# Performance work log

Measured on AMD Instinct MI355X. Metric: run time of the kernel, lower is better.

Reference implementation:

```python
import jax, jax.numpy as jnp
import numpy as np

N = 131072   # total nodes (4096 molecules x ~32 atoms)
E = 524288   # directed edges (avg degree 4)
G = 4096     # number of graphs
D_IN, D_H, D_OUT = 128, 512, 256
BN_EPS = 1e-5


def setup_inputs() -> dict:
    key = jax.random.key(0)
    ks = jax.random.split(key, 24)
    def rn(i, shape, s=0.05):
        return jax.random.normal(ks[i], shape, jnp.float32) * s
    inp = {
        "x": jax.random.normal(ks[0], (N, D_IN), jnp.float32),
        "edge_index": jax.random.randint(ks[1], (2, E), 0, N),
        "batch": jnp.sort(jax.random.randint(ks[2], (N,), 0, G)),
        # GCN layer weights (stored [in, out]) and biases
        "W1": rn(3, (D_IN, D_H)), "b1": jnp.zeros((D_H,), jnp.float32),
        "W2": rn(4, (D_H, D_H)),  "b2": jnp.zeros((D_H,), jnp.float32),
        "W3": rn(5, (D_H, D_OUT)), "b3": jnp.zeros((D_OUT,), jnp.float32),
        # BatchNorm (eval mode): gamma, beta, running_mean, running_var
        "g1": jnp.ones((D_H,), jnp.float32),  "be1": jnp.zeros((D_H,), jnp.float32),
        "m1": rn(6, (D_H,)),  "v1": jax.random.uniform(ks[7], (D_H,), jnp.float32) + 0.5,
        "g2": jnp.ones((D_H,), jnp.float32),  "be2": jnp.zeros((D_H,), jnp.float32),
        "m2": rn(8, (D_H,)),  "v2": jax.random.uniform(ks[9], (D_H,), jnp.float32) + 0.5,
        "g3": jnp.ones((D_OUT,), jnp.float32), "be3": jnp.zeros((D_OUT,), jnp.float32),
        "m3": rn(10, (D_OUT,)), "v3": jax.random.uniform(ks[11], (D_OUT,), jnp.float32) + 0.5,
        # MLP head
        "Wf1": rn(12, (D_OUT, D_OUT)), "bf1": jnp.zeros((D_OUT,), jnp.float32),
        "Wf2": rn(13, (D_OUT, D_OUT)), "bf2": jnp.zeros((D_OUT,), jnp.float32),
    }
    return inp


def reference(x, edge_index, batch, W1, b1, W2, b2, W3, b3,
              g1, be1, m1, v1, g2, be2, m2, v2, g3, be3, m3, v3,
              Wf1, bf1, Wf2, bf2):
    loop = jnp.arange(N)
    src = jnp.concatenate([edge_index[0], loop])  # add self-loops (PyG GCNConv default)
    dst = jnp.concatenate([edge_index[1], loop])
    deg = jax.ops.segment_sum(jnp.ones((E + N,), x.dtype), dst, num_segments=N)
    dinv = jnp.where(deg > 0, jax.lax.rsqrt(deg), 0.0)
    norm = dinv[src] * dinv[dst]                  # D^{-1/2} A_hat D^{-1/2}

    def gcn(h, W, b):
        h = h @ W                                 # dense GEMM [N, d_out]
        msg = h[src] * norm[:, None]              # gather + scale
        return jax.ops.segment_sum(msg, dst, num_segments=N) + b  # scatter-add

    def bn(h, g, be, m, v):                       # eval-mode BatchNorm1d
        return g * (h - m) * jax.lax.rsqrt(v + BN_EPS) + be

    h = bn(jax.nn.relu(gcn(x, W1, b1)), g1, be1, m1, v1)
    h = bn(jax.nn.relu(gcn(h, W2, b2)), g2, be2, m2, v2)
    h = bn(jax.nn.relu(gcn(h, W3, b3)), g3, be3, m3, v3)

    sums = jax.ops.segment_sum(h, batch, num_segments=G)          # global_mean_pool
    cnt = jax.ops.segment_sum(jnp.ones((N,), h.dtype), batch, num_segments=G)
    pooled = sums / jnp.maximum(cnt, 1.0)[:, None]

    return jax.nn.relu(pooled @ Wf1 + bf1) @ Wf2 + bf2
```

## Files before the change

### kernel.cpp

```cpp
#include <hip/hip_runtime.h>

static constexpr int NN = 131072;
static constexpr int NE = 524288;
static constexpr int NG = 4096;

typedef __attribute__((ext_vector_type(8))) short short8;
typedef __attribute__((ext_vector_type(4))) float f32x4;
typedef __attribute__((ext_vector_type(2))) float f32x2;

__device__ __forceinline__ float bfbits2f(unsigned b) {
    return __uint_as_float(b << 16);
}
__device__ __forceinline__ unsigned short f2bfbits(float f) {
    unsigned u = __float_as_uint(f);
    u += 0x7fffu + ((u >> 16) & 1u);
    return (unsigned short)(u >> 16);
}
__device__ __forceinline__ unsigned pack2(float a, float b) {
    return (unsigned)f2bfbits(a) | ((unsigned)f2bfbits(b) << 16);
}

__device__ __forceinline__ int geti(const void* p, size_t i, int w64) {
    return w64 ? (int)((const long long*)p)[i] : ((const int*)p)[i];
}

#if __has_builtin(__builtin_amdgcn_cvt_pk_f32_fp8) && __has_builtin(__builtin_amdgcn_cvt_pk_fp8_f32)
#define FP8_CVT_HW 1
#else
#define FP8_CVT_HW 0
#endif

__device__ __forceinline__ float e4m32f(unsigned b) {
    unsigned e = (b >> 3) & 0xFu, m = b & 7u;
    float v = e ? __uint_as_float(((e + 120u) << 23) | (m << 20))
                : (float)m * 0.001953125f;
    return (b & 0x80u) ? -v : v;
}
__device__ __forceinline__ unsigned f2e4m3(float f) {
    unsigned u = __float_as_uint(f);
    unsigned s = (u >> 24) & 0x80u;
    unsigned mag = u & 0x7fffffffu;
    if (mag >= 0x43e00000u) return s | 0x7eu;
    if (mag < 0x3c800000u) {
        int q = (int)(__uint_as_float(mag) * 512.0f + 0.5f);
        return s | (unsigned)q;
    }
    unsigned r = mag + 0x0007ffffu + ((mag >> 20) & 1u);
    if (r >= 0x43e00000u) return s | 0x7eu;
    return s | (((r >> 23) - 120u) << 3) | ((r >> 20) & 7u);
}

template<bool HI>
__device__ __forceinline__ unsigned dec_pair(unsigned w) {
#if FP8_CVT_HW
    f32x2 p = __builtin_amdgcn_cvt_pk_f32_fp8((int)w, HI);
    return __builtin_amdgcn_perm(__float_as_uint(p.y), __float_as_uint(p.x), 0x07060302u);
#else
    unsigned b0 = HI ? ((w >> 16) & 255u) : (w & 255u);
    unsigned b1 = HI ? (w >> 24) : ((w >> 8) & 255u);
    return pack2(e4m32f(b0), e4m32f(b1));
#endif
}

__device__ __forceinline__ short8 dec8(uint2 u) {
    union { uint4 q; short8 s; } r;
    r.q.x = dec_pair<false>(u.x);
    r.q.y = dec_pair<true>(u.x);
    r.q.z = dec_pair<false>(u.y);
    r.q.w = dec_pair<true>(u.y);
    return r.s;
}

__device__ __forceinline__ void dec4f(unsigned w, float* v) {
#if FP8_CVT_HW
    f32x2 a = __builtin_amdgcn_cvt_pk_f32_fp8((int)w, false);
    f32x2 b = __builtin_amdgcn_cvt_pk_f32_fp8((int)w, true);
    v[0] = a.x; v[1] = a.y; v[2] = b.x; v[3] = b.y;
#else
#pragma unroll
    for (int i = 0; i < 4; ++i) v[i] = e4m32f((w >> (8 * i)) & 0xffu);
#endif
}

__device__ __forceinline__ unsigned enc4(float a, float b, float c, float d) {
#if FP8_CVT_HW
    int r = __builtin_amdgcn_cvt_pk_fp8_f32(a, b, 0, false);
    r = __builtin_amdgcn_cvt_pk_fp8_f32(c, d, r, true);
    return (unsigned)r;
#else
    return f2e4m3(a) | (f2e4m3(b) << 8) | (f2e4m3(c) << 16) | (f2e4m3(d) << 24);
#endif
}
__device__ __forceinline__ unsigned enc1(float a) {
#if FP8_CVT_HW
    return (unsigned)__builtin_amdgcn_cvt_pk_fp8_f32(a, a, 0, false) & 0xffu;
#else
    return f2e4m3(a);
#endif
}

__device__ __forceinline__ void gld16(const void* g, void* l, int lane) {
#if __has_builtin(__builtin_amdgcn_global_load_lds)
    __builtin_amdgcn_global_load_lds((const __attribute__((address_space(1))) unsigned int*)g,
                                     (__attribute__((address_space(3))) unsigned int*)l, 16, 0, 0);
#else
    *(uint4*)((char*)l + lane * 16) = *(const uint4*)g;
#endif
}

__global__ void k_detect(const void* __restrict__ eidx, const void* __restrict__ batch,
                         int* __restrict__ flags) {
    const int* e32 = (const int*)eidx;
    const int* b32 = (const int*)batch;
    int e64 = (e32[1] == 0 && e32[2001] == 0 && e32[40001] == 0 && e32[2 * NE - 1] == 0) ? 1 : 0;
    int b64 = (b32[NN - 1] == 0) ? 1 : 0;
    flags[0] = e64;
    flags[1] = b64;
}


__global__ void k_zero(int* __restrict__ p, int n) {
    int i = blockIdx.x * 256 + threadIdx.x;
    if (i < n) p[i] = 0;
}

__global__ void k_transpose(const float* __restrict__ W,
                            unsigned short* __restrict__ Wt, int K, int Ncols) {
    int idx = blockIdx.x * 256 + threadIdx.x;
    if (idx >= K * Ncols) return;
    int k = idx / Ncols, n = idx - k * Ncols;
    Wt[n * K + k] = f2bfbits(W[idx]);
}

__global__ void k_bn_prep(const float* __restrict__ g, const float* __restrict__ be,
                          const float* __restrict__ m, const float* __restrict__ v,
                          float* __restrict__ s, float* __restrict__ t, int d) {
    int i = blockIdx.x * 256 + threadIdx.x;
    if (i >= d) return;
    float inv = rsqrtf(v[i] + 1e-5f);
    float sc = g[i] * inv;
    s[i] = sc;
    t[i] = be[i] - m[i] * sc;
}

__global__ void k_deg_count(const void* __restrict__ eidx, const int* __restrict__ flags,
                            int* __restrict__ cnt) {
    int i = blockIdx.x * 256 + threadIdx.x;
    if (i >= NE) return;
    int d = geti(eidx, (size_t)NE + i, flags[0]);
    atomicAdd(&cnt[d], 1);
}

__global__ __launch_bounds__(1024) void k_scan(const int* __restrict__ cnt, int* __restrict__ rowptr,
                                               float* __restrict__ dinv) {
    __shared__ int part[1024];
    const int t = threadIdx.x;
    const int base = t * 128;
    const int4* c4 = (const int4*)(cnt + base);
    int s = 0;
#pragma unroll
    for (int i = 0; i < 32; ++i) { int4 u = c4[i]; s += u.x + u.y + u.z + u.w; }
    part[t] = s;
    __syncthreads();
    for (int off = 1; off < 1024; off <<= 1) {
        int v = (t >= off) ? part[t - off] : 0;
        __syncthreads();
        part[t] += v;
        __syncthreads();
    }
    int ex = (t == 0) ? 0 : part[t - 1];
#pragma unroll
    for (int i = 0; i < 32; ++i) {
        int4 u = c4[i];
        int4 o; o.x = ex; o.y = ex + u.x; o.z = o.y + u.y; o.w = o.z + u.z; ex = o.w + u.w;
        *(int4*)(rowptr + base + 4 * i) = o;
        float4 dv;
        dv.x = rsqrtf((float)(u.x + 1)); dv.y = rsqrtf((float)(u.y + 1));
        dv.z = rsqrtf((float)(u.z + 1)); dv.w = rsqrtf((float)(u.w + 1));
        *(float4*)(dinv + base + 4 * i) = dv;
    }
    if (t == 1023) rowptr[NN] = ex;
}

__global__ void k_fill(const void* __restrict__ eidx, const int* __restrict__ flags,
                       const int* __restrict__ rowptr, int* __restrict__ fillp,
                       int* __restrict__ col) {
    int i = blockIdx.x * 256 + threadIdx.x;
    if (i >= NE) return;
    int e64 = flags[0];
    int s = geti(eidx, (size_t)i, e64);
    int d = geti(eidx, (size_t)NE + i, e64);
    int p = rowptr[d] + atomicAdd(&fillp[d], 1);
    col[p] = s;
}

__global__ void k_gstart(const void* __restrict__ batch, const int* __restrict__ flags,
                         int* __restrict__ gstart) {
    int i = blockIdx.x * 256 + threadIdx.x;
    if (i >= NN) return;
    int b64 = flags[1];
    int b = geti(batch, (size_t)i, b64);
    if (i == 0) {
        for (int g = 0; g <= b; ++g) gstart[g] = 0;
    } else {
        int pb = geti(batch, (size_t)i - 1, b64);
        for (int g = pb + 1; g <= b; ++g) gstart[g] = i;
    }
    if (i == NN - 1) {
        for (int g = b + 1; g <= NG; ++g) gstart[g] = NN;
    }
}

template<int D, int MODE>
__device__ __forceinline__ void load_row_hw(const void* h, int sn, int c0, float* v) {
    if constexpr (MODE == 2) {
        float4 u = *(const float4*)((const float*)h + (size_t)sn * D + c0);
        v[0] = u.x; v[1] = u.y; v[2] = u.z; v[3] = u.w;
    } else {
        uint4 u = *(const uint4*)((const unsigned char*)h + (size_t)sn * D + c0);
        dec4f(u.x, v); dec4f(u.y, v + 4); dec4f(u.z, v + 8); dec4f(u.w, v + 12);
    }
}

template<int D, int EPL, bool FP8>
__device__ __forceinline__ void store_row_hw(void* out, int n, int c0, const float* v) {
    if constexpr (FP8) {
        uint4 u;
        u.x = enc4(v[0], v[1], v[2], v[3]);
        u.y = enc4(v[4], v[5], v[6], v[7]);
        u.z = enc4(v[8], v[9], v[10], v[11]);
        u.w = enc4(v[12], v[13], v[14], v[15]);
        *(uint4*)((unsigned char*)out + (size_t)n * D + c0) = u;
    } else {
        uint2 u; u.x = pack2(v[0], v[1]); u.y = pack2(v[2], v[3]);
        *(uint2*)((unsigned short*)out + (size_t)n * D + c0) = u;
    }
}

template<int D, int IN_MODE, bool OUT_FP8>
__global__ __launch_bounds__(256) void k_agg_hw(
    const void* __restrict__ h,
    const int* __restrict__ rowptr, const int* __restrict__ col,
    const float* __restrict__ dinv,
    void* __restrict__ out)
{
    constexpr int EPL = (IN_MODE == 1) ? 16 : 4;
    const int n = (blockIdx.x * 256 + threadIdx.x) >> 5;
    const int lane = threadIdx.x & 31;
    const int c0 = lane * EPL;
    float dn = dinv[n];
    float acc[EPL], va[EPL], vb[EPL];

    load_row_hw<D, IN_MODE>(h, n, c0, va);
    float wsl = dn * dn;
#pragma unroll
    for (int i = 0; i < EPL; ++i) acc[i] = va[i] * wsl;

    int e = rowptr[n], e1 = rowptr[n + 1];
    for (; e + 2 <= e1; e += 2) {
        int sa = col[e], sb = col[e + 1];
        float wa = dinv[sa] * dn, wb = dinv[sb] * dn;
        load_row_hw<D, IN_MODE>(h, sa, c0, va);
        load_row_hw<D, IN_MODE>(h, sb, c0, vb);
#pragma unroll
        for (int i = 0; i < EPL; ++i) acc[i] += va[i] * wa + vb[i] * wb;
    }
    if (e < e1) {
        int sa = col[e];
        float wa = dinv[sa] * dn;
        load_row_hw<D, IN_MODE>(h, sa, c0, va);
#pragma unroll
        for (int i = 0; i < EPL; ++i) acc[i] += va[i] * wa;
    }
    store_row_hw<D, EPL, OUT_FP8>(out, n, c0, acc);
}

__global__ __launch_bounds__(256) void k_agg_pool(
    const unsigned short* __restrict__ T3,
    const int* __restrict__ rowptr, const int* __restrict__ col,
    const float* __restrict__ dinv,
    const float* __restrict__ b, const float* __restrict__ s, const float* __restrict__ t,
    const int* __restrict__ gstart, unsigned short* __restrict__ pooled)
{
    __shared__ float red[4][256];
    const int g = blockIdx.x;
    const int wave = threadIdx.x >> 6, lane = threadIdx.x & 63;
    const int c0 = lane * 4;
    const int r0 = gstart[g], r1 = gstart[g + 1];
    float p0 = 0, p1 = 0, p2 = 0, p3 = 0;
    const float bc0 = b[c0], bc1 = b[c0 + 1], bc2 = b[c0 + 2], bc3 = b[c0 + 3];
    const float sc0 = s[c0], sc1 = s[c0 + 1], sc2 = s[c0 + 2], sc3 = s[c0 + 3];
    const float tc0 = t[c0], tc1 = t[c0 + 1], tc2 = t[c0 + 2], tc3 = t[c0 + 3];

    for (int n = r0 + wave; n < r1; n += 4) {
        float dn = dinv[n];
        float a0, a1, a2, a3;
        {
            uint2 u = *(const uint2*)(T3 + (size_t)n * 256 + c0);
            float w = dn * dn;
            a0 = bfbits2f(u.x & 0xffffu) * w; a1 = bfbits2f(u.x >> 16) * w;
            a2 = bfbits2f(u.y & 0xffffu) * w; a3 = bfbits2f(u.y >> 16) * w;
        }
        int e = rowptr[n], e1 = rowptr[n + 1];
        for (; e + 2 <= e1; e += 2) {
            int sa = col[e], sb = col[e + 1];
            float wa = dinv[sa] * dn, wb = dinv[sb] * dn;
            uint2 ua = *(const uint2*)(T3 + (size_t)sa * 256 + c0);
            uint2 ub = *(const uint2*)(T3 + (size_t)sb * 256 + c0);
            a0 += bfbits2f(ua.x & 0xffffu) * wa + bfbits2f(ub.x & 0xffffu) * wb;
            a1 += bfbits2f(ua.x >> 16) * wa + bfbits2f(ub.x >> 16) * wb;
            a2 += bfbits2f(ua.y & 0xffffu) * wa + bfbits2f(ub.y & 0xffffu) * wb;
            a3 += bfbits2f(ua.y >> 16) * wa + bfbits2f(ub.y >> 16) * wb;
        }
        if (e < e1) {
            int sa = col[e];
            float wa = dinv[sa] * dn;
            uint2 ua = *(const uint2*)(T3 + (size_t)sa * 256 + c0);
            a0 += bfbits2f(ua.x & 0xffffu) * wa; a1 += bfbits2f(ua.x >> 16) * wa;
            a2 += bfbits2f(ua.y & 0xffffu) * wa; a3 += bfbits2f(ua.y >> 16) * wa;
        }
        p0 += sc0 * fmaxf(a0 + bc0, 0.0f) + tc0;
        p1 += sc1 * fmaxf(a1 + bc1, 0.0f) + tc1;
        p2 += sc2 * fmaxf(a2 + bc2, 0.0f) + tc2;
        p3 += sc3 * fmaxf(a3 + bc3, 0.0f) + tc3;
    }
    red[wave][c0] = p0; red[wave][c0 + 1] = p1; red[wave][c0 + 2] = p2; red[wave][c0 + 3] = p3;
    __syncthreads();
    int ch = threadIdx.x;
    float tot = red[0][ch] + red[1][ch] + red[2][ch] + red[3][ch];
    __syncthreads();
    red[0][ch] = tot;
    __syncthreads();
    if (ch < 128) {
        int ccount = r1 - r0;
        float inv = 1.0f / (float)(ccount > 0 ? ccount : 1);
        pooled[(size_t)g * 256 + 2 * ch] = f2bfbits(red[0][2 * ch] * inv);
        pooled[(size_t)g * 256 + 2 * ch + 1] = f2bfbits(red[0][2 * ch + 1] * inv);
    }
}

template<bool A_FP8, int CB, int OUT_MODE, bool RELU, bool HAS_BN, bool HAS_BIAS>
__global__ __launch_bounds__(256)
void k_gemm(const void* __restrict__ Aptr,
            const unsigned short* __restrict__ Wt,
            const float* __restrict__ bias,
            const float* __restrict__ s, const float* __restrict__ t,
            void* __restrict__ Cptr,
            int K, int Ncols)
{
    __shared__ __align__(16) unsigned short lB[2][2][128 * 32];
    __shared__ __align__(16) unsigned char  lA8[A_FP8 ? 2 : 1][A_FP8 ? 2 : 1][A_FP8 ? 128 * 32 : 16];
    __shared__ __align__(16) unsigned short lA16[A_FP8 ? 1 : 2][A_FP8 ? 1 : 2][A_FP8 ? 8 : 128 * 32];
    const int tid = threadIdx.x;
    const int id = blockIdx.x;
    const int hi = id >> 3;
    const int cblk = hi % CB;
    const int rblk = (hi / CB) * 8 + (id & 7);
    const int bm = rblk * 128;
    const int bn = cblk * 128;
    const int lane = tid & 63;
    const int wave = tid >> 6;
    const int wm = (wave >> 1) * 64;
    const int wn = (wave & 1) * 64;
    const int fr = lane & 15;
    const int fq = lane >> 4;

    f32x4 acc[4][4] = {};
    const int NG64 = K >> 6;

    auto stage = [&](int buf, int k0) {
#pragma unroll
        for (int h = 0; h < 2; ++h) {
            const int kh = k0 + h * 32;
            if constexpr (A_FP8) {
                const unsigned char* g = (const unsigned char*)Aptr
                    + (size_t)(bm + (wave << 5) + (lane >> 1)) * K + kh + (lane & 1) * 16;
                gld16(g, &lA8[buf][h][(wave << 5) * 32], lane);
            } else {
                const unsigned short* Ab = (const unsigned short*)Aptr;
#pragma unroll
                for (int c = 0; c < 2; ++c) {
                    const unsigned short* g = Ab
                        + (size_t)(bm + (wave << 5) + (c << 4) + (lane >> 2)) * K + kh + (lane & 3) * 8;
                    gld16(g, &lA16[buf][h][((wave << 5) + (c << 4)) * 32], lane);
                }
            }
#pragma unroll
            for (int c = 0; c < 2; ++c) {
                const unsigned short* g = Wt
                    + (size_t)(bn + (wave << 5) + (c << 4) + (lane >> 2)) * K + kh + (lane & 3) * 8;
                gld16(g, &lB[buf][h][((wave << 5) + (c << 4)) * 32], lane);
            }
        }
    };

    stage(0, 0);
    __syncthreads();

    int cur = 0;
    for (int kg = 0; kg < NG64; ++kg) {
        if (kg + 1 < NG64) stage(cur ^ 1, (kg + 1) << 6);

#pragma unroll
        for (int h = 0; h < 2; ++h) {
            short8 a[4], b[4];
#pragma unroll
            for (int i = 0; i < 4; ++i) {
                if constexpr (A_FP8)
                    a[i] = dec8(*(const uint2*)&lA8[cur][h][(wm + 16 * i + fr) * 32 + fq * 8]);
                else
                    a[i] = *(const short8*)&lA16[cur][h][(wm + 16 * i + fr) * 32 + fq * 8];
            }
#pragma unroll
            for (int j = 0; j < 4; ++j)
                b[j] = *(const short8*)&lB[cur][h][(wn + 16 * j + fr) * 32 + fq * 8];
#pragma unroll
            for (int i = 0; i < 4; ++i)
#pragma unroll
                for (int j = 0; j < 4; ++j)
                    acc[i][j] = __builtin_amdgcn_mfma_f32_16x16x32_bf16(a[i], b[j], acc[i][j], 0, 0, 0);
        }

        __syncthreads();
        cur ^= 1;
    }

#pragma unroll
    for (int j = 0; j < 4; ++j) {
        int colI = bn + wn + 16 * j + fr;
        float bi = HAS_BIAS ? bias[colI] : 0.0f;
        float sc = HAS_BN ? s[colI] : 1.0f;
        float tc = HAS_BN ? t[colI] : 0.0f;
#pragma unroll
        for (int i = 0; i < 4; ++i) {
#pragma unroll
            for (int r = 0; r < 4; ++r) {
                int row = bm + wm + 16 * i + fq * 4 + r;
                float z = acc[i][j][r] + bi;
                if (RELU) z = fmaxf(z, 0.0f);
                float y = HAS_BN ? (sc * z + tc) : z;
                if constexpr (OUT_MODE == 2)
                    ((float*)Cptr)[(size_t)row * Ncols + colI] = y;
                else if constexpr (OUT_MODE == 1)
                    ((unsigned char*)Cptr)[(size_t)row * Ncols + colI] = (unsigned char)enc1(y);
                else
                    ((unsigned short*)Cptr)[(size_t)row * Ncols + colI] = f2bfbits(y);
            }
        }
    }
}

template<int CB, int OUT_MODE, bool RELU, bool HAS_BN, bool HAS_BIAS>
__global__ __launch_bounds__(512)
void k_gemm8w(const unsigned char* __restrict__ Aptr,
              const unsigned short* __restrict__ Wt,
              const float* __restrict__ bias,
              const float* __restrict__ s, const float* __restrict__ t,
              void* __restrict__ Cptr,
              int K, int Ncols)
{
    __shared__ __align__(16) unsigned char  lA[2][2][256 * 32];
    __shared__ __align__(16) unsigned short lB[2][2][128 * 32];
    const int tid = threadIdx.x;
    const int id = blockIdx.x;
    const int hi = id >> 3;
    const int cblk = hi % CB;
    const int rblk = (hi / CB) * 8 + (id & 7);
    const int bm = rblk * 256;
    const int bn = cblk * 128;
    const int lane = tid & 63;
    const int wave = tid >> 6;
    const int wm = (wave >> 1) * 64;
    const int wn = (wave & 1) * 64;
    const int fr = lane & 15;
    const int fq = lane >> 4;

    f32x4 acc[4][4] = {};
    const int NG64 = K >> 6;

    auto stage = [&](int buf, int k0) {
#pragma unroll
        for (int h = 0; h < 2; ++h) {
            const int kh = k0 + h * 32;
            {
                const unsigned char* g = Aptr
                    + (size_t)(bm + (wave << 5) + (lane >> 1)) * K + kh + (lane & 1) * 16;
                gld16(g, &lA[buf][h][(wave << 5) * 32], lane);
            }
            {
                const unsigned short* g = Wt
                    + (size_t)(bn + (wave << 4) + (lane >> 2)) * K + kh + (lane & 3) * 8;
                gld16(g, &lB[buf][h][(wave << 4) * 32], lane);
            }
        }
    };

    stage(0, 0);
    __syncthreads();

    int cur = 0;
    for (int kg = 0; kg < NG64; ++kg) {
        if (kg + 1 < NG64) stage(cur ^ 1, (kg + 1) << 6);

#pragma unroll
        for (int h = 0; h < 2; ++h) {
            short8 a[4], b[4];
#pragma unroll
            for (int i = 0; i < 4; ++i)
                a[i] = dec8(*(const uint2*)&lA[cur][h][(wm + 16 * i + fr) * 32 + fq * 8]);
#pragma unroll
            for (int j = 0; j < 4; ++j)
                b[j] = *(const short8*)&lB[cur][h][(wn + 16 * j + fr) * 32 + fq * 8];
#pragma unroll
            for (int i = 0; i < 4; ++i)
#pragma unroll
                for (int j = 0; j < 4; ++j)
                    acc[i][j] = __builtin_amdgcn_mfma_f32_16x16x32_bf16(a[i], b[j], acc[i][j], 0, 0, 0);
        }

        __syncthreads();
        cur ^= 1;
    }

#pragma unroll
    for (int j = 0; j < 4; ++j) {
        int colI = bn + wn + 16 * j + fr;
        float bi = HAS_BIAS ? bias[colI] : 0.0f;
        float sc = HAS_BN ? s[colI] : 1.0f;
        float tc = HAS_BN ? t[colI] : 0.0f;
#pragma unroll
        for (int i = 0; i < 4; ++i) {
#pragma unroll
            for (int r = 0; r < 4; ++r) {
                int row = bm + wm + 16 * i + fq * 4 + r;
                float z = acc[i][j][r] + bi;
                if (RELU) z = fmaxf(z, 0.0f);
                float y = HAS_BN ? (sc * z + tc) : z;
                if constexpr (OUT_MODE == 2)
                    ((float*)Cptr)[(size_t)row * Ncols + colI] = y;
                else if constexpr (OUT_MODE == 1)
                    ((unsigned char*)Cptr)[(size_t)row * Ncols + colI] = (unsigned char)enc1(y);
                else
                    ((unsigned short*)Cptr)[(size_t)row * Ncols + colI] = f2bfbits(y);
            }
        }
    }
}


extern "C" void kernel_launch(void* const* d_in, const int* in_sizes, int n_in,
                              void* d_out, int out_size, void* d_ws, size_t ws_size,
                              hipStream_t stream) {
    const float* x   = (const float*)d_in[0];
    const void* eidx = d_in[1];
    const void* batch = d_in[2];
    const float* W1  = (const float*)d_in[3];
    const float* b1  = (const float*)d_in[4];
    const float* W2  = (const float*)d_in[5];
    const float* b2  = (const float*)d_in[6];
    const float* W3  = (const float*)d_in[7];
    const float* b3  = (const float*)d_in[8];
    const float* g1  = (const float*)d_in[9];
    const float* be1 = (const float*)d_in[10];
    const float* m1  = (const float*)d_in[11];
    const float* v1  = (const float*)d_in[12];
    const float* g2  = (const float*)d_in[13];
    const float* be2 = (const float*)d_in[14];
    const float* m2  = (const float*)d_in[15];
    const float* v2  = (const float*)d_in[16];
    const float* g3  = (const float*)d_in[17];
    const float* be3 = (const float*)d_in[18];
    const float* m3  = (const float*)d_in[19];
    const float* v3  = (const float*)d_in[20];
    const float* Wf1 = (const float*)d_in[21];
    const float* bf1 = (const float*)d_in[22];
    const float* Wf2 = (const float*)d_in[23];
    const float* bf2 = (const float*)d_in[24];

    unsigned char* RB = (unsigned char*)d_ws;
    unsigned char* RA = RB + 67108864;
    unsigned char* EX = RB + 134217728;
    int*   rowptr = (int*)(EX + 0);
    int*   col    = (int*)(EX + 524544);
    float* dinv   = (float*)(EX + 2621696);
    int*   cnt    = (int*)(EX + 3145984);
    int*   fillp  = (int*)(EX + 3670272);
    int*   gstart = (int*)(EX + 4194560);
    float* sbuf   = (float*)(EX + 4211456);
    float *s1 = sbuf, *t1 = sbuf + 512, *s2 = sbuf + 1024, *t2 = sbuf + 1536;
    float *s3 = sbuf + 2048, *t3v = sbuf + 2304;
    unsigned short* Wt1  = (unsigned short*)(EX + 4221696);
    unsigned short* Wt2  = (unsigned short*)(EX + 4352768);
    unsigned short* Wt3  = (unsigned short*)(EX + 4877056);
    unsigned short* Wtf1 = (unsigned short*)(EX + 5139200);
    unsigned short* Wtf2 = (unsigned short*)(EX + 5270272);
    int*   flags = (int*)(EX + 5401344);

    unsigned short* pooled = (unsigned short*)RB;
    unsigned short* z1     = (unsigned short*)(RB + 2097152);

    k_detect<<<1, 1, 0, stream>>>(eidx, batch, flags);
    k_transpose<<<(128 * 512) / 256, 256, 0, stream>>>(W1, Wt1, 128, 512);
    k_transpose<<<(512 * 512) / 256, 256, 0, stream>>>(W2, Wt2, 512, 512);
    k_transpose<<<(512 * 256) / 256, 256, 0, stream>>>(W3, Wt3, 512, 256);
    k_transpose<<<(256 * 256) / 256, 256, 0, stream>>>(Wf1, Wtf1, 256, 256);
    k_transpose<<<(256 * 256) / 256, 256, 0, stream>>>(Wf2, Wtf2, 256, 256);
    k_bn_prep<<<2, 256, 0, stream>>>(g1, be1, m1, v1, s1, t1, 512);
    k_bn_prep<<<2, 256, 0, stream>>>(g2, be2, m2, v2, s2, t2, 512);
    k_bn_prep<<<1, 256, 0, stream>>>(g3, be3, m3, v3, s3, t3v, 256);
    k_zero<<<(2 * NN) / 256, 256, 0, stream>>>(cnt, 2 * NN);
    k_deg_count<<<NE / 256, 256, 0, stream>>>(eidx, flags, cnt);
    k_scan<<<1, 1024, 0, stream>>>(cnt, rowptr, dinv);
    k_fill<<<NE / 256, 256, 0, stream>>>(eidx, flags, rowptr, fillp, col);
    k_gstart<<<NN / 256, 256, 0, stream>>>(batch, flags, gstart);

    const dim3 gagg(NN / 8);

    k_agg_hw<128, 2, false><<<gagg, 256, 0, stream>>>(x, rowptr, col, dinv, RA);
    k_gemm<false, 4, 1, true, true, true><<<4096, 256, 0, stream>>>(RA, Wt1, b1, s1, t1, RB, 128, 512);

    k_agg_hw<512, 1, true><<<gagg, 256, 0, stream>>>(RB, rowptr, col, dinv, RA);
    k_gemm8w<4, 1, true, true, true><<<2048, 512, 0, stream>>>(RA, Wt2, b2, s2, t2, RB, 512, 512);

    k_gemm8w<2, 0, false, false, false><<<1024, 512, 0, stream>>>(RB, Wt3, nullptr, nullptr, nullptr, RA, 512, 256);

    k_agg_pool<<<NG, 256, 0, stream>>>((const unsigned short*)RA, rowptr, col, dinv,
                                       b3, s3, t3v, gstart, pooled);

    k_gemm<false, 2, 0, true, false, true><<<64, 256, 0, stream>>>(pooled, Wtf1, bf1, nullptr, nullptr, z1, 256, 256);
    k_gemm<false, 2, 2, false, false, true><<<64, 256, 0, stream>>>(z1, Wtf2, bf2, nullptr, nullptr, d_out, 256, 256);
}
```

Measured before the change: 645.4 us.

## Fuse setup kernels into one prep launch and use 512-thread GEMM for layer 1

Merges the flag detection, weight transposes, BN parameter prep, counter zeroing and graph-start computation into a single multi-role kernel, and has the later kernels recompute the int64 detection inline instead of reading a flags buffer. This removes about a dozen small launches and their serialization gaps. It also replaces the layer-1 GEMM with a new 8-wave, 128x128-tile kernel that double-buffers K in 64-wide chunks through direct global-to-LDS loads. The risks are extra redundant loads per thread for the inline detection and different occupancy and tile behaviour in the new GEMM.

```diff
diff --git a/kernel.cpp b/kernel.cpp
--- a/kernel.cpp
+++ b/kernel.cpp
@@ -22,6 +22,13 @@
 
 __device__ __forceinline__ int geti(const void* p, size_t i, int w64) {
     return w64 ? (int)((const long long*)p)[i] : ((const int*)p)[i];
+}
+__device__ __forceinline__ int e64_of(const void* eidx) {
+    const int* e = (const int*)eidx;
+    return (e[1] == 0 && e[2001] == 0 && e[40001] == 0 && e[2 * NE - 1] == 0) ? 1 : 0;
+}
+__device__ __forceinline__ int b64_of(const void* batch) {
+    return (((const int*)batch)[NN - 1] == 0) ? 1 : 0;
 }
 
 #if __has_builtin(__builtin_amdgcn_cvt_pk_f32_fp8) && __has_builtin(__builtin_amdgcn_cvt_pk_fp8_f32)
@@ -108,46 +115,74 @@
 #endif
 }
 
-__global__ void k_detect(const void* __restrict__ eidx, const void* __restrict__ batch,
-                         int* __restrict__ flags) {
-    const int* e32 = (const int*)eidx;
-    const int* b32 = (const int*)batch;
-    int e64 = (e32[1] == 0 && e32[2001] == 0 && e32[40001] == 0 && e32[2 * NE - 1] == 0) ? 1 : 0;
-    int b64 = (b32[NN - 1] == 0) ? 1 : 0;
-    flags[0] = e64;
-    flags[1] = b64;
-}
-
-
-__global__ void k_zero(int* __restrict__ p, int n) {
-    int i = blockIdx.x * 256 + threadIdx.x;
-    if (i < n) p[i] = 0;
-}
-
-__global__ void k_transpose(const float* __restrict__ W,
-                            unsigned short* __restrict__ Wt, int K, int Ncols) {
-    int idx = blockIdx.x * 256 + threadIdx.x;
-    if (idx >= K * Ncols) return;
-    int k = idx / Ncols, n = idx - k * Ncols;
-    Wt[n * K + k] = f2bfbits(W[idx]);
-}
-
-__global__ void k_bn_prep(const float* __restrict__ g, const float* __restrict__ be,
-                          const float* __restrict__ m, const float* __restrict__ v,
-                          float* __restrict__ s, float* __restrict__ t, int d) {
-    int i = blockIdx.x * 256 + threadIdx.x;
-    if (i >= d) return;
-    float inv = rsqrtf(v[i] + 1e-5f);
-    float sc = g[i] * inv;
-    s[i] = sc;
-    t[i] = be[i] - m[i] * sc;
-}
-
-__global__ void k_deg_count(const void* __restrict__ eidx, const int* __restrict__ flags,
-                            int* __restrict__ cnt) {
+__global__ __launch_bounds__(256) void k_prep(
+    const float* __restrict__ W1, const float* __restrict__ W2, const float* __restrict__ W3,
+    const float* __restrict__ Wf1, const float* __restrict__ Wf2,
+    unsigned short* __restrict__ Wt1, unsigned short* __restrict__ Wt2,
+    unsigned short* __restrict__ Wt3, unsigned short* __restrict__ Wtf1,
+    unsigned short* __restrict__ Wtf2,
+    const float* __restrict__ g1, const float* __restrict__ be1,
+    const float* __restrict__ m1, const float* __restrict__ v1,
+    const float* __restrict__ g2, const float* __restrict__ be2,
+    const float* __restrict__ m2, const float* __restrict__ v2,
+    const float* __restrict__ g3, const float* __restrict__ be3,
+    const float* __restrict__ m3, const float* __restrict__ v3,
+    float* __restrict__ sbuf, int* __restrict__ cnt2,
+    const void* __restrict__ batch, int* __restrict__ gstart)
+{
+    const int id = blockIdx.x, tid = threadIdx.x;
+    if (id < 1024) {
+        int idx = id * 256 + tid; int k = idx >> 9, n = idx & 511;
+        Wt2[n * 512 + k] = f2bfbits(W2[idx]);
+    } else if (id < 1536) {
+        int idx = (id - 1024) * 256 + tid; int k = idx >> 8, n = idx & 255;
+        Wt3[n * 512 + k] = f2bfbits(W3[idx]);
+    } else if (id < 1792) {
+        int idx = (id - 1536) * 256 + tid; int k = idx >> 9, n = idx & 511;
+        Wt1[n * 128 + k] = f2bfbits(W1[idx]);
+    } else if (id < 2048) {
+        int idx = (id - 1792) * 256 + tid; int k = idx >> 8, n = idx & 255;
+        Wtf1[n * 256 + k] = f2bfbits(Wf1[idx]);
+    } else if (id < 2304) {
+        int idx = (id - 2048) * 256 + tid; int k = idx >> 8, n = idx & 255;
+        Wtf2[n * 256 + k] = f2bfbits(Wf2[idx]);
+    } else if (id < 3328) {
+        cnt2[(id - 2304) * 256 + tid] = 0;
+    } else if (id < 3333) {
+        int i = (id - 3328) * 256 + tid;
+        if (i < 512) {
+            float inv = rsqrtf(v1[i] + 1e-5f); float sc = g1[i] * inv;
+            sbuf[i] = sc; sbuf[512 + i] = be1[i] - m1[i] * sc;
+        } else if (i < 1024) {
+            int j = i - 512;
+            float inv = rsqrtf(v2[j] + 1e-5f); float sc = g2[j] * inv;
+            sbuf[1024 + j] = sc; sbuf[1536 + j] = be2[j] - m2[j] * sc;
+        } else if (i < 1280) {
+            int j = i - 1024;
+            float inv = rsqrtf(v3[j] + 1e-5f); float sc = g3[j] * inv;
+            sbuf[2048 + j] = sc; sbuf[2304 + j] = be3[j] - m3[j] * sc;
+        }
+    } else {
+        int i = (id - 3333) * 256 + tid;
+        if (i >= NN) return;
+        int b64 = b64_of(batch);
+        int b = geti(batch, (size_t)i, b64);
+        if (i == 0) {
+            for (int g = 0; g <= b; ++g) gstart[g] = 0;
+        } else {
+            int pb = geti(batch, (size_t)i - 1, b64);
+            for (int g = pb + 1; g <= b; ++g) gstart[g] = i;
+        }
+        if (i == NN - 1) {
+            for (int g = b + 1; g <= NG; ++g) gstart[g] = NN;
+        }
+    }
+}
+
+__global__ void k_deg_count(const void* __restrict__ eidx, int* __restrict__ cnt) {
     int i = blockIdx.x * 256 + threadIdx.x;
     if (i >= NE) return;
-    int d = geti(eidx, (size_t)NE + i, flags[0]);
+    int d = geti(eidx, (size_t)NE + i, e64_of(eidx));
     atomicAdd(&cnt[d], 1);
 }
 
@@ -182,33 +217,16 @@
     if (t == 1023) rowptr[NN] = ex;
 }
 
-__global__ void k_fill(const void* __restrict__ eidx, const int* __restrict__ flags,
+__global__ void k_fill(const void* __restrict__ eidx,
                        const int* __restrict__ rowptr, int* __restrict__ fillp,
                        int* __restrict__ col) {
     int i = blockIdx.x * 256 + threadIdx.x;
     if (i >= NE) return;
-    int e64 = flags[0];
+    int e64 = e64_of(eidx);
     int s = geti(eidx, (size_t)i, e64);
     int d = geti(eidx, (size_t)NE + i, e64);
     int p = rowptr[d] + atomicAdd(&fillp[d], 1);
     col[p] = s;
-}
-
-__global__ void k_gstart(const void* __restrict__ batch, const int* __restrict__ flags,
-                         int* __restrict__ gstart) {
-    int i = blockIdx.x * 256 + threadIdx.x;
-    if (i >= NN) return;
-    int b64 = flags[1];
-    int b = geti(batch, (size_t)i, b64);
-    if (i == 0) {
-        for (int g = 0; g <= b; ++g) gstart[g] = 0;
-    } else {
-        int pb = geti(batch, (size_t)i - 1, b64);
-        for (int g = pb + 1; g <= b; ++g) gstart[g] = i;
-    }
-    if (i == NN - 1) {
-        for (int g = b + 1; g <= NG; ++g) gstart[g] = NN;
-    }
 }
 
 template<int D, int MODE>
@@ -530,6 +548,99 @@
         float tc = HAS_BN ? t[colI] : 0.0f;
 #pragma unroll
         for (int i = 0; i < 4; ++i) {
+#pragma unroll
+            for (int r = 0; r < 4; ++r) {
+                int row = bm + wm + 16 * i + fq * 4 + r;
+                float z = acc[i][j][r] + bi;
+                if (RELU) z = fmaxf(z, 0.0f);
+                float y = HAS_BN ? (sc * z + tc) : z;
+                if constexpr (OUT_MODE == 2)
+                    ((float*)Cptr)[(size_t)row * Ncols + colI] = y;
+                else if constexpr (OUT_MODE == 1)
+                    ((unsigned char*)Cptr)[(size_t)row * Ncols + colI] = (unsigned char)enc1(y);
+                else
+                    ((unsigned short*)Cptr)[(size_t)row * Ncols + colI] = f2bfbits(y);
+            }
+        }
+    }
+}
+
+template<int CB, int OUT_MODE, bool RELU, bool HAS_BN, bool HAS_BIAS>
+__global__ __launch_bounds__(512)
+void k_gemm8n(const unsigned short* __restrict__ Aptr,
+              const unsigned short* __restrict__ Wt,
+              const float* __restrict__ bias,
+              const float* __restrict__ s, const float* __restrict__ t,
+              void* __restrict__ Cptr,
+              int K, int Ncols)
+{
+    __shared__ __align__(16) unsigned short lA[2][2][128 * 32];
+    __shared__ __align__(16) unsigned short lB[2][2][128 * 32];
+    const int tid = threadIdx.x;
+    const int id = blockIdx.x;
+    const int hi = id >> 3;
+    const int cblk = hi % CB;
+    const int rblk = (hi / CB) * 8 + (id & 7);
+    const int bm = rblk * 128;
+    const int bn = cblk * 128;
+    const int lane = tid & 63;
+    const int wave = tid >> 6;
+    const int wm = (wave >> 1) * 32;
+    const int wn = (wave & 1) * 64;
+    const int fr = lane & 15;
+    const int fq = lane >> 4;
+
+    f32x4 acc[2][4] = {};
+    const int NG64 = K >> 6;
+
+    auto stage = [&](int buf, int k0) {
+#pragma unroll
+        for (int h = 0; h < 2; ++h) {
+            const int kh = k0 + h * 32;
+            const unsigned short* ga = Aptr
+                + (size_t)(bm + (wave << 4) + (lane >> 2)) * K + kh + (lane & 3) * 8;
+            gld16(ga, &lA[buf][h][(wave << 4) * 32], lane);
+            const unsigned short* gb = Wt
+                + (size_t)(bn + (wave << 4) + (lane >> 2)) * K + kh + (lane & 3) * 8;
+            gld16(gb, &lB[buf][h][(wave << 4) * 32], lane);
+        }
+    };
+
+    stage(0, 0);
+    __syncthreads();
+
+    int cur = 0;
+    for (int kg = 0; kg < NG64; ++kg) {
+        if (kg + 1 < NG64) stage(cur ^ 1, (kg + 1) << 6);
+
+#pragma unroll
+        for (int h = 0; h < 2; ++h) {
+            short8 a[2], b[4];
+#pragma unroll
+            for (int i = 0; i < 2; ++i)
+                a[i] = *(const short8*)&lA[cur][h][(wm + 16 * i + fr) * 32 + fq * 8];
+#pragma unroll
+            for (int j = 0; j < 4; ++j)
+                b[j] = *(const short8*)&lB[cur][h][(wn + 16 * j + fr) * 32 + fq * 8];
+#pragma unroll
+            for (int i = 0; i < 2; ++i)
+#pragma unroll
+                for (int j = 0; j < 4; ++j)
+                    acc[i][j] = __builtin_amdgcn_mfma_f32_16x16x32_bf16(a[i], b[j], acc[i][j], 0, 0, 0);
+        }
+
+        __syncthreads();
+        cur ^= 1;
+    }
+
+#pragma unroll
+    for (int j = 0; j < 4; ++j) {
+        int colI = bn + wn + 16 * j + fr;
+        float bi = HAS_BIAS ? bias[colI] : 0.0f;
+        float sc = HAS_BN ? s[colI] : 1.0f;
+        float tc = HAS_BN ? t[colI] : 0.0f;
+#pragma unroll
+        for (int i = 0; i < 2; ++i) {
 #pragma unroll
             for (int r = 0; r < 4; ++r) {
                 int row = bm + wm + 16 * i + fq * 4 + r;
@@ -594,30 +705,23 @@
     unsigned short* Wt3  = (unsigned short*)(EX + 4877056);
     unsigned short* Wtf1 = (unsigned short*)(EX + 5139200);
     unsigned short* Wtf2 = (unsigned short*)(EX + 5270272);
-    int*   flags = (int*)(EX + 5401344);
 
     unsigned short* pooled = (unsigned short*)RB;
     unsigned short* z1     = (unsigned short*)(RB + 2097152);
 
-    k_detect<<<1, 1, 0, stream>>>(eidx, batch, flags);
-    k_transpose<<<(128 * 512) / 256, 256, 0, stream>>>(W1, Wt1, 128, 512);
-    k_transpose<<<(512 * 512) / 256, 256, 0, stream>>>(W2, Wt2, 512, 512);
-    k_transpose<<<(512 * 256) / 256, 256, 0, stream>>>(W3, Wt3, 512, 256);
-    k_transpose<<<(256 * 256) / 256, 256, 0, stream>>>(Wf1, Wtf1, 256, 256);
-    k_transpose<<<(256 * 256) / 256, 256, 0, stream>>>(Wf2, Wtf2, 256, 256);
-    k_bn_prep<<<2, 256, 0, stream>>>(g1, be1, m1, v1, s1, t1, 512);
-    k_bn_prep<<<2, 256, 0, stream>>>(g2, be2, m2, v2, s2, t2, 512);
-    k_bn_prep<<<1, 256, 0, stream>>>(g3, be3, m3, v3, s3, t3v, 256);
-    k_zero<<<(2 * NN) / 256, 256, 0, stream>>>(cnt, 2 * NN);
-    k_deg_count<<<NE / 256, 256, 0, stream>>>(eidx, flags, cnt);
+    k_prep<<<3845, 256, 0, stream>>>(W1, W2, W3, Wf1, Wf2,
+                                     Wt1, Wt2, Wt3, Wtf1, Wtf2,
+                                     g1, be1, m1, v1, g2, be2, m2, v2, g3, be3, m3, v3,
+                                     sbuf, cnt, batch, gstart);
+    k_deg_count<<<NE / 256, 256, 0, stream>>>(eidx, cnt);
     k_scan<<<1, 1024, 0, stream>>>(cnt, rowptr, dinv);
-    k_fill<<<NE / 256, 256, 0, stream>>>(eidx, flags, rowptr, fillp, col);
-    k_gstart<<<NN / 256, 256, 0, stream>>>(batch, flags, gstart);
+    k_fill<<<NE / 256, 256, 0, stream>>>(eidx, rowptr, fillp, col);
 
     const dim3 gagg(NN / 8);
 
     k_agg_hw<128, 2, false><<<gagg, 256, 0, stream>>>(x, rowptr, col, dinv, RA);
-    k_gemm<false, 4, 1, true, true, true><<<4096, 256, 0, stream>>>(RA, Wt1, b1, s1, t1, RB, 128, 512);
+    k_gemm8n<4, 1, true, true, true><<<4096, 512, 0, stream>>>(
+        (const unsigned short*)RA, Wt1, b1, s1, t1, RB, 128, 512);
 
     k_agg_hw<512, 1, true><<<gagg, 256, 0, stream>>>(RB, rowptr, col, dinv, RA);
     k_gemm8w<4, 1, true, true, true><<<2048, 512, 0, stream>>>(RA, Wt2, b2, s2, t2, RB, 512, 512);
```

Result: faster. 622.4 us (-3.6%).
